# Kernel optimization log

Hardware: AMD Instinct MI355X
Metric: run time of the kernel (lower is better)

Reference implementation:

```python
import jax, jax.numpy as jnp
import numpy as np

EPS = 1e-8
B, H, N, W = 128, 4, 4096, 128


def setup_inputs() -> dict:
    key = jax.random.key(0)
    k1, k2, k3 = jax.random.split(key, 3)
    memory = jax.random.normal(k1, (B, N, W), dtype=jnp.float32)
    controls = jax.random.normal(k2, (B, H * (3 * W + 6)), dtype=jnp.float32)
    write_dist_bias = jax.random.normal(k3, (1, H, N), dtype=jnp.float32) * 10.0
    return {"memory": memory, "controls": controls, "write_dist_bias": write_dist_bias}


def _split_controls(controls):
    # split_tensor: sequential narrows along last dim, each part viewed as [B, H, size]
    sizes = [W, W, W, 1, 1, 3, 1]
    parts, pos = [], 0
    for s in sizes:
        parts.append(controls[:, pos:pos + H * s].reshape(B, H, s))
        pos += H * s
    return parts  # keys, erase, write, betas, gates, shifts, gammas


def _circular_convolution(weights, shifts):
    # out[n] = s0*w[n-1] + s1*w[n] + s2*w[n+1]  (circular)
    return (shifts[..., 0:1] * jnp.roll(weights, 1, axis=-1)
            + shifts[..., 1:2] * weights
            + shifts[..., 2:3] * jnp.roll(weights, -1, axis=-1))


def reference(memory, controls, write_dist_bias):
    keys_r, erase_r, write_r, betas_r, gates_r, shifts_r, gammas_r = _split_controls(controls)

    keys = jnp.tanh(keys_r)                      # [B,H,W]
    betas = jax.nn.softplus(betas_r)             # [B,H,1]
    gates = jax.nn.sigmoid(gates_r)              # [B,H,1]
    shifts = jax.nn.softmax(shifts_r, axis=-1)   # [B,H,3]
    gammas = 1.0 + jax.nn.softplus(gammas_r)     # [B,H,1]

    # cosine distance: [B,H,N]
    dots = jnp.einsum('bnw,bhw->bhn', memory, keys)
    norm = jnp.linalg.norm(keys, axis=-1)[:, :, None] * jnp.linalg.norm(memory, axis=-1)[:, None, :]
    scores = dots / (norm + EPS)

    w_content = jax.nn.softmax(scores * betas, axis=-1)

    # prev weights: first step -> softmax of bias broadcast over batch
    prev_weights = jax.nn.softmax(jnp.broadcast_to(write_dist_bias, (B, H, N)), axis=-1)

    w_interp = gates * w_content + (1.0 - gates) * prev_weights
    w_shift = _circular_convolution(w_interp, shifts)
    w_sharp = w_shift ** gammas
    write_dist = w_sharp / (jnp.sum(w_sharp, axis=-1, keepdims=True) + EPS)  # [B,H,N]

    write_data = jnp.tanh(write_r)        # [B,H,W]
    erase_data = jax.nn.sigmoid(erase_r)  # [B,H,W]

    # erase matrix: prod over heads of (1 - dist x erase) -> [B,N,W]
    erase_matrix = jnp.prod(1.0 - write_dist[:, :, :, None] * erase_data[:, :, None, :], axis=1)
    update_matrix = jnp.einsum('bhn,bhw->bnw', write_dist, write_data)
    return memory * erase_matrix + update_matrix
```

## Files before the change

### kernel.cpp

```cpp
#include <hip/hip_runtime.h>
#include <math.h>

#define B 128
#define H 4
#define N 4096
#define W 128
#define CTRL (H*(3*W+6))
#define EPSF 1e-8f

typedef float f32x4 __attribute__((ext_vector_type(4)));

__device__ __forceinline__ float sigmoidf_(float x){ return 1.0f/(1.0f+expf(-x)); }
__device__ __forceinline__ float softplusf_(float x){ return (x>20.0f)? x : log1pf(expf(x)); }
__device__ __forceinline__ float pospowf_(float t, float g){ return exp2f(g * log2f(t)); }

__device__ __forceinline__ float blockReduceSum256(float v, float* red){
  int tid = threadIdx.x;
  #pragma unroll
  for (int off=32; off>0; off>>=1) v += __shfl_xor(v, off);
  __syncthreads();
  if ((tid&63)==0) red[tid>>6] = v;
  __syncthreads();
  return red[0]+red[1]+red[2]+red[3];
}
__device__ __forceinline__ float blockReduceMax256(float v, float* red){
  int tid = threadIdx.x;
  #pragma unroll
  for (int off=32; off>0; off>>=1) v = fmaxf(v, __shfl_xor(v, off));
  __syncthreads();
  if ((tid&63)==0) red[tid>>6] = v;
  __syncthreads();
  return fmaxf(fmaxf(red[0],red[1]), fmaxf(red[2],red[3]));
}

__global__ __launch_bounds__(128) void prep_kernel(const float* __restrict__ controls,
    float* __restrict__ keys_t, float* __restrict__ erase_s, float* __restrict__ write_t,
    float* __restrict__ scal, const float* __restrict__ bias, float* __restrict__ pw){
  int bid = blockIdx.x;
  int tid = threadIdx.x;
  if (bid >= B*H){
    int h = bid - B*H;
    __shared__ float red2[2];
    const float4* brow = (const float4*)(bias + (size_t)h*N);
    float4 p[8]; float lm = -1e30f;
    #pragma unroll
    for (int j=0;j<8;j++){
      p[j] = brow[tid + 128*j];
      lm = fmaxf(lm, fmaxf(fmaxf(p[j].x,p[j].y), fmaxf(p[j].z,p[j].w)));
    }
    #pragma unroll
    for (int off=32; off>0; off>>=1) lm = fmaxf(lm, __shfl_xor(lm, off));
    if ((tid&63)==0) red2[tid>>6] = lm;
    __syncthreads();
    float m = fmaxf(red2[0], red2[1]);
    float ls = 0.0f;
    #pragma unroll
    for (int j=0;j<8;j++){
      p[j].x = expf(p[j].x-m); p[j].y = expf(p[j].y-m);
      p[j].z = expf(p[j].z-m); p[j].w = expf(p[j].w-m);
      ls += p[j].x+p[j].y+p[j].z+p[j].w;
    }
    #pragma unroll
    for (int off=32; off>0; off>>=1) ls += __shfl_xor(ls, off);
    __syncthreads();
    if ((tid&63)==0) red2[tid>>6] = ls;
    __syncthreads();
    float inv = 1.0f/(red2[0]+red2[1]);
    float4* orow = (float4*)(pw + (size_t)h*N);
    #pragma unroll
    for (int j=0;j<8;j++)
      orow[tid + 128*j] = make_float4(p[j].x*inv, p[j].y*inv, p[j].z*inv, p[j].w*inv);
    return;
  }
  int b = bid >> 2, h = bid & (H-1);
  int w = tid;
  const float* c = controls + (size_t)b*CTRL;
  float k = tanhf(c[h*W + w]);
  keys_t [bid*W + w] = k;
  erase_s[bid*W + w] = sigmoidf_(c[1*H*W + h*W + w]);
  write_t[bid*W + w] = tanhf   (c[2*H*W + h*W + w]);
  __shared__ float red[128];
  red[w] = k*k;
  __syncthreads();
  for (int s=64; s>0; s>>=1){ if (w<s) red[w] += red[w+s]; __syncthreads(); }
  if (w==0){
    float knorm = sqrtf(red[0]);
    float beta  = softplusf_(c[3*H*W + h]);
    float gate  = sigmoidf_ (c[3*H*W + H + h]);
    float s0r = c[3*H*W + 2*H + h*3 + 0];
    float s1r = c[3*H*W + 2*H + h*3 + 1];
    float s2r = c[3*H*W + 2*H + h*3 + 2];
    float mm = fmaxf(s0r, fmaxf(s1r, s2r));
    float e0 = expf(s0r-mm), e1 = expf(s1r-mm), e2 = expf(s2r-mm);
    float inv = 1.0f/(e0+e1+e2);
    float gamma = 1.0f + softplusf_(c[3*H*W + 5*H + h]);
    float* sc = scal + bid*8;
    sc[0]=beta; sc[1]=gate; sc[2]=e0*inv; sc[3]=e1*inv; sc[4]=e2*inv; sc[5]=gamma; sc[6]=knorm;
  }
}

__global__ __launch_bounds__(256) void scores_kernel(const float* __restrict__ memory,
    const float* __restrict__ keys_t, const float* __restrict__ scal,
    float* __restrict__ scores){
  int b = blockIdx.y;
  int n0 = blockIdx.x * 64;
  int tid = threadIdx.x;
  int grp = tid >> 4, l16 = tid & 15;
  __shared__ __align__(16) float kk[H][W];
  __shared__ float kbeta[H], kn[H];
  for (int i = tid; i < H*W; i += 256) kk[0][i] = keys_t[(size_t)b*H*W + i];
  if (tid < H){ kbeta[tid] = scal[(b*H+tid)*8 + 0]; kn[tid] = scal[(b*H+tid)*8 + 6]; }
  __syncthreads();
  float4 ka[H], kb[H];
  #pragma unroll
  for (int h=0;h<H;h++){
    ka[h] = *(const float4*)&kk[h][l16*8];
    kb[h] = *(const float4*)&kk[h][l16*8+4];
  }
  float beta_l = (l16 < H) ? kbeta[l16] : 0.0f;
  float kn_l   = (l16 < H) ? kn[l16]    : 1.0f;
  #pragma unroll
  for (int it=0; it<4; ++it){
    int n = n0 + it*16 + grp;
    const float4* mp = (const float4*)(memory + ((size_t)b*N + n)*W + l16*8);
    float4 ma = mp[0], mb = mp[1];
    float msq = ma.x*ma.x+ma.y*ma.y+ma.z*ma.z+ma.w*ma.w
              + mb.x*mb.x+mb.y*mb.y+mb.z*mb.z+mb.w*mb.w;
    float d0 = ma.x*ka[0].x+ma.y*ka[0].y+ma.z*ka[0].z+ma.w*ka[0].w
             + mb.x*kb[0].x+mb.y*kb[0].y+mb.z*kb[0].z+mb.w*kb[0].w;
    float d1 = ma.x*ka[1].x+ma.y*ka[1].y+ma.z*ka[1].z+ma.w*ka[1].w
             + mb.x*kb[1].x+mb.y*kb[1].y+mb.z*kb[1].z+mb.w*kb[1].w;
    float d2 = ma.x*ka[2].x+ma.y*ka[2].y+ma.z*ka[2].z+ma.w*ka[2].w
             + mb.x*kb[2].x+mb.y*kb[2].y+mb.z*kb[2].z+mb.w*kb[2].w;
    float d3 = ma.x*ka[3].x+ma.y*ka[3].y+ma.z*ka[3].z+ma.w*ka[3].w
             + mb.x*kb[3].x+mb.y*kb[3].y+mb.z*kb[3].z+mb.w*kb[3].w;
    #pragma unroll
    for (int off=1; off<16; off<<=1){
      msq += __shfl_xor(msq, off);
      d0  += __shfl_xor(d0 , off);
      d1  += __shfl_xor(d1 , off);
      d2  += __shfl_xor(d2 , off);
      d3  += __shfl_xor(d3 , off);
    }
    if (l16 < H){
      float dd = (l16==0)?d0 : (l16==1)?d1 : (l16==2)?d2 : d3;
      float mn = sqrtf(msq);
      scores[((size_t)(b*H + l16))*N + n] = beta_l*dd/(kn_l*mn + EPSF);
    }
  }
}

__global__ __launch_bounds__(256) void dist_kernel(const float* scores,
    const float* __restrict__ pw, const float* __restrict__ scal, float* wd){
  int bh = blockIdx.x;
  int h = bh & (H-1);
  int tid = threadIdx.x;
  __shared__ __align__(16) float buf[N];
  __shared__ float red[4];
  const float4* srow4 = (const float4*)(scores + (size_t)bh*N);

  float4 v[4]; float lmax = -1e30f;
  #pragma unroll
  for (int j=0;j<4;j++){
    v[j] = srow4[tid + 256*j];
    lmax = fmaxf(lmax, fmaxf(fmaxf(v[j].x,v[j].y), fmaxf(v[j].z,v[j].w)));
  }
  float smax = blockReduceMax256(lmax, red);
  float lsum = 0.0f;
  #pragma unroll
  for (int j=0;j<4;j++){
    v[j].x = expf(v[j].x-smax); v[j].y = expf(v[j].y-smax);
    v[j].z = expf(v[j].z-smax); v[j].w = expf(v[j].w-smax);
    lsum += v[j].x+v[j].y+v[j].z+v[j].w;
  }
  float ssum = blockReduceSum256(lsum, red);

  float gate = scal[bh*8+1];
  float ga = gate/ssum, gb = 1.0f - gate;
  const float4* prow4 = (const float4*)(pw + (size_t)h*N);
  #pragma unroll
  for (int j=0;j<4;j++){
    float4 p = prow4[tid + 256*j];
    float4 o;
    o.x = ga*v[j].x + gb*p.x;  o.y = ga*v[j].y + gb*p.y;
    o.z = ga*v[j].z + gb*p.z;  o.w = ga*v[j].w + gb*p.w;
    ((float4*)buf)[tid + 256*j] = o;
  }
  __syncthreads();

  float s0 = scal[bh*8+2], s1 = scal[bh*8+3], s2 = scal[bh*8+4], gamma = scal[bh*8+5];
  float4 q[4]; float qsum = 0.0f;
  #pragma unroll
  for (int j=0;j<4;j++){
    int m = 4*(tid + 256*j);
    float4 c = *(const float4*)&buf[m];
    float wm = buf[(m + N - 1) & (N-1)];
    float wp = buf[(m + 4) & (N-1)];
    float t0 = s0*wm  + s1*c.x + s2*c.y;
    float t1 = s0*c.x + s1*c.y + s2*c.z;
    float t2 = s0*c.y + s1*c.z + s2*c.w;
    float t3 = s0*c.z + s1*c.w + s2*wp;
    q[j].x = pospowf_(t0, gamma); q[j].y = pospowf_(t1, gamma);
    q[j].z = pospowf_(t2, gamma); q[j].w = pospowf_(t3, gamma);
    qsum += q[j].x+q[j].y+q[j].z+q[j].w;
  }
  float tot = blockReduceSum256(qsum, red);
  float inv = 1.0f/(tot + EPSF);
  float4* wrow4 = (float4*)(wd + (size_t)bh*N);
  #pragma unroll
  for (int j=0;j<4;j++)
    wrow4[tid + 256*j] = make_float4(q[j].x*inv, q[j].y*inv, q[j].z*inv, q[j].w*inv);
}

__global__ __launch_bounds__(256) void final_kernel(const float* __restrict__ memory,
    const float* __restrict__ wd, const float* __restrict__ erase_s,
    const float* __restrict__ write_t, float* __restrict__ out){
  int b  = (B-1) - blockIdx.y;
  int n0 = ((N/64-1) - blockIdx.x) * 64;
  int tid = threadIdx.x;
  __shared__ __align__(16) float esh[H][W];
  __shared__ __align__(16) float wsh[H][W];
  __shared__ float wdsh[H][64];
  for (int i=tid;i<H*W;i+=256){ esh[0][i] = erase_s[(size_t)b*H*W+i]; wsh[0][i] = write_t[(size_t)b*H*W+i]; }
  for (int i=tid;i<H*64;i+=256){ int h=i>>6, r=i&63; wdsh[h][r] = wd[((size_t)(b*H+h))*N + n0 + r]; }
  __syncthreads();
  int wq = (tid & 31) * 4;
  int rl = tid >> 5;
  #pragma unroll
  for (int rr = 0; rr < 8; ++rr){
    int r = rl + rr*8;
    int n = n0 + r;
    size_t base = ((size_t)b*N + n)*W + wq;
    f32x4 m = __builtin_nontemporal_load((const f32x4*)(memory + base));
    float px=1.f, py=1.f, pz=1.f, pwv=1.f;
    float ux=0.f, uy=0.f, uz=0.f, uw=0.f;
    #pragma unroll
    for (int h=0;h<H;h++){
      float d = wdsh[h][r];
      float4 e  = *(const float4*)&esh[h][wq];
      float4 wv = *(const float4*)&wsh[h][wq];
      px *= 1.0f - d*e.x;  py *= 1.0f - d*e.y;
      pz *= 1.0f - d*e.z;  pwv*= 1.0f - d*e.w;
      ux += d*wv.x;  uy += d*wv.y;  uz += d*wv.z;  uw += d*wv.w;
    }
    f32x4 o;
    o.x = m.x*px + ux;  o.y = m.y*py + uy;
    o.z = m.z*pz + uz;  o.w = m.w*pwv + uw;
    __builtin_nontemporal_store(o, (f32x4*)(out + base));
  }
}

extern "C" void kernel_launch(void* const* d_in, const int* in_sizes, int n_in,
                              void* d_out, int out_size, void* d_ws, size_t ws_size,
                              hipStream_t stream){
  const float* memory   = (const float*)d_in[0];
  const float* controls = (const float*)d_in[1];
  const float* bias     = (const float*)d_in[2];
  float* out = (float*)d_out;

  float* ws      = (float*)d_ws;
  float* keys_t  = ws;
  float* erase_s = keys_t  + B*H*W;
  float* write_t = erase_s + B*H*W;
  float* scal    = write_t + B*H*W;
  float* pw      = scal    + B*H*8;
  float* scores  = pw      + H*N;
  float* wd      = scores;

  prep_kernel  <<<dim3(B*H + H),  dim3(128), 0, stream>>>(controls, keys_t, erase_s, write_t, scal, bias, pw);
  scores_kernel<<<dim3(N/64, B),  dim3(256), 0, stream>>>(memory, keys_t, scal, scores);
  dist_kernel  <<<dim3(B*H),      dim3(256), 0, stream>>>(scores, pw, scal, wd);
  final_kernel <<<dim3(N/64, B),  dim3(256), 0, stream>>>(memory, wd, erase_s, write_t, out);
}
```

Before: 498.5 us.

## Fuse write-distribution and memory-update kernels into one 1024-thread kernel

Merges dist_kernel and final_kernel into one kernel launched on a grid of 2 by B blocks of 1024 threads. Each block recomputes the full write distribution for all four heads of its batch in shared memory (64KB) and then updates half of the memory rows. This removes one launch and the global write and read of the distribution, at the cost of doing the softmax, shift and sharpen work twice per batch. It also cuts the grid to 256 large blocks, which may limit occupancy and latency hiding during the bandwidth-bound update phase.

```diff
diff --git a/kernel.cpp b/kernel.cpp
--- a/kernel.cpp
+++ b/kernel.cpp
@@ -14,23 +14,29 @@
 __device__ __forceinline__ float softplusf_(float x){ return (x>20.0f)? x : log1pf(expf(x)); }
 __device__ __forceinline__ float pospowf_(float t, float g){ return exp2f(g * log2f(t)); }
 
-__device__ __forceinline__ float blockReduceSum256(float v, float* red){
+__device__ __forceinline__ float blockReduceSum1024(float v, float* red){
   int tid = threadIdx.x;
   #pragma unroll
   for (int off=32; off>0; off>>=1) v += __shfl_xor(v, off);
   __syncthreads();
   if ((tid&63)==0) red[tid>>6] = v;
   __syncthreads();
-  return red[0]+red[1]+red[2]+red[3];
-}
-__device__ __forceinline__ float blockReduceMax256(float v, float* red){
+  float s = 0.0f;
+  #pragma unroll
+  for (int i=0;i<16;i++) s += red[i];
+  return s;
+}
+__device__ __forceinline__ float blockReduceMax1024(float v, float* red){
   int tid = threadIdx.x;
   #pragma unroll
   for (int off=32; off>0; off>>=1) v = fmaxf(v, __shfl_xor(v, off));
   __syncthreads();
   if ((tid&63)==0) red[tid>>6] = v;
   __syncthreads();
-  return fmaxf(fmaxf(red[0],red[1]), fmaxf(red[2],red[3]));
+  float s = -1e30f;
+  #pragma unroll
+  for (int i=0;i<16;i++) s = fmaxf(s, red[i]);
+  return s;
 }
 
 __global__ __launch_bounds__(128) void prep_kernel(const float* __restrict__ controls,
@@ -150,102 +156,87 @@
   }
 }
 
-__global__ __launch_bounds__(256) void dist_kernel(const float* scores,
-    const float* __restrict__ pw, const float* __restrict__ scal, float* wd){
-  int bh = blockIdx.x;
-  int h = bh & (H-1);
-  int tid = threadIdx.x;
-  __shared__ __align__(16) float buf[N];
-  __shared__ float red[4];
-  const float4* srow4 = (const float4*)(scores + (size_t)bh*N);
-
-  float4 v[4]; float lmax = -1e30f;
-  #pragma unroll
-  for (int j=0;j<4;j++){
-    v[j] = srow4[tid + 256*j];
-    lmax = fmaxf(lmax, fmaxf(fmaxf(v[j].x,v[j].y), fmaxf(v[j].z,v[j].w)));
-  }
-  float smax = blockReduceMax256(lmax, red);
-  float lsum = 0.0f;
-  #pragma unroll
-  for (int j=0;j<4;j++){
-    v[j].x = expf(v[j].x-smax); v[j].y = expf(v[j].y-smax);
-    v[j].z = expf(v[j].z-smax); v[j].w = expf(v[j].w-smax);
-    lsum += v[j].x+v[j].y+v[j].z+v[j].w;
-  }
-  float ssum = blockReduceSum256(lsum, red);
-
-  float gate = scal[bh*8+1];
-  float ga = gate/ssum, gb = 1.0f - gate;
-  const float4* prow4 = (const float4*)(pw + (size_t)h*N);
-  #pragma unroll
-  for (int j=0;j<4;j++){
-    float4 p = prow4[tid + 256*j];
+__global__ __launch_bounds__(1024) void fused_kernel(const float* __restrict__ memory,
+    const float* __restrict__ scores, const float* __restrict__ pw,
+    const float* __restrict__ scal, const float* __restrict__ erase_s,
+    const float* __restrict__ write_t, float* __restrict__ out){
+  int b = (B-1) - blockIdx.y;
+  int q = blockIdx.x;
+  int tid = threadIdx.x;
+  __shared__ float wd_sh[H][N];
+  __shared__ __align__(16) float esh[H][W];
+  __shared__ __align__(16) float wsh[H][W];
+  __shared__ float red[16];
+  for (int i=tid;i<H*W;i+=1024){
+    esh[0][i] = erase_s[(size_t)b*H*W+i];
+    wsh[0][i] = write_t[(size_t)b*H*W+i];
+  }
+
+  #pragma unroll
+  for (int h=0; h<H; h++){
+    const float4* srow = (const float4*)(scores + ((size_t)(b*H+h))*N);
+    float4 v = srow[tid];
+    float lm = fmaxf(fmaxf(v.x,v.y), fmaxf(v.z,v.w));
+    float smax = blockReduceMax1024(lm, red);
+    v.x = expf(v.x-smax); v.y = expf(v.y-smax);
+    v.z = expf(v.z-smax); v.w = expf(v.w-smax);
+    float ssum = blockReduceSum1024(v.x+v.y+v.z+v.w, red);
+    float gate = scal[(b*H+h)*8+1];
+    float ga = gate/ssum, gb = 1.0f - gate;
+    float4 p = ((const float4*)(pw + (size_t)h*N))[tid];
     float4 o;
-    o.x = ga*v[j].x + gb*p.x;  o.y = ga*v[j].y + gb*p.y;
-    o.z = ga*v[j].z + gb*p.z;  o.w = ga*v[j].w + gb*p.w;
-    ((float4*)buf)[tid + 256*j] = o;
-  }
-  __syncthreads();
-
-  float s0 = scal[bh*8+2], s1 = scal[bh*8+3], s2 = scal[bh*8+4], gamma = scal[bh*8+5];
-  float4 q[4]; float qsum = 0.0f;
-  #pragma unroll
-  for (int j=0;j<4;j++){
-    int m = 4*(tid + 256*j);
-    float4 c = *(const float4*)&buf[m];
-    float wm = buf[(m + N - 1) & (N-1)];
-    float wp = buf[(m + 4) & (N-1)];
+    o.x = ga*v.x + gb*p.x;  o.y = ga*v.y + gb*p.y;
+    o.z = ga*v.z + gb*p.z;  o.w = ga*v.w + gb*p.w;
+    ((float4*)wd_sh[h])[tid] = o;
+  }
+  __syncthreads();
+
+  #pragma unroll
+  for (int h=0; h<H; h++){
+    float s0 = scal[(b*H+h)*8+2], s1 = scal[(b*H+h)*8+3];
+    float s2 = scal[(b*H+h)*8+4], g  = scal[(b*H+h)*8+5];
+    int m = 4*tid;
+    float4 c = *(const float4*)&wd_sh[h][m];
+    float wm = wd_sh[h][(m + N - 1) & (N-1)];
+    float wp = wd_sh[h][(m + 4) & (N-1)];
     float t0 = s0*wm  + s1*c.x + s2*c.y;
     float t1 = s0*c.x + s1*c.y + s2*c.z;
     float t2 = s0*c.y + s1*c.z + s2*c.w;
     float t3 = s0*c.z + s1*c.w + s2*wp;
-    q[j].x = pospowf_(t0, gamma); q[j].y = pospowf_(t1, gamma);
-    q[j].z = pospowf_(t2, gamma); q[j].w = pospowf_(t3, gamma);
-    qsum += q[j].x+q[j].y+q[j].z+q[j].w;
-  }
-  float tot = blockReduceSum256(qsum, red);
-  float inv = 1.0f/(tot + EPSF);
-  float4* wrow4 = (float4*)(wd + (size_t)bh*N);
-  #pragma unroll
-  for (int j=0;j<4;j++)
-    wrow4[tid + 256*j] = make_float4(q[j].x*inv, q[j].y*inv, q[j].z*inv, q[j].w*inv);
-}
-
-__global__ __launch_bounds__(256) void final_kernel(const float* __restrict__ memory,
-    const float* __restrict__ wd, const float* __restrict__ erase_s,
-    const float* __restrict__ write_t, float* __restrict__ out){
-  int b  = (B-1) - blockIdx.y;
-  int n0 = ((N/64-1) - blockIdx.x) * 64;
-  int tid = threadIdx.x;
-  __shared__ __align__(16) float esh[H][W];
-  __shared__ __align__(16) float wsh[H][W];
-  __shared__ float wdsh[H][64];
-  for (int i=tid;i<H*W;i+=256){ esh[0][i] = erase_s[(size_t)b*H*W+i]; wsh[0][i] = write_t[(size_t)b*H*W+i]; }
-  for (int i=tid;i<H*64;i+=256){ int h=i>>6, r=i&63; wdsh[h][r] = wd[((size_t)(b*H+h))*N + n0 + r]; }
-  __syncthreads();
-  int wq = (tid & 31) * 4;
-  int rl = tid >> 5;
-  #pragma unroll
-  for (int rr = 0; rr < 8; ++rr){
-    int r = rl + rr*8;
-    int n = n0 + r;
-    size_t base = ((size_t)b*N + n)*W + wq;
+    float q0 = pospowf_(t0,g), q1 = pospowf_(t1,g);
+    float q2 = pospowf_(t2,g), q3 = pospowf_(t3,g);
+    float tot = blockReduceSum1024(q0+q1+q2+q3, red);
+    float inv = 1.0f/(tot + EPSF);
+    *(float4*)&wd_sh[h][m] = make_float4(q0*inv, q1*inv, q2*inv, q3*inv);
+  }
+  __syncthreads();
+
+  int col = tid & 31;
+  int rg  = tid >> 5;
+  f32x4 ev[H], wv[H];
+  #pragma unroll
+  for (int h=0;h<H;h++){
+    ev[h] = *(const f32x4*)&esh[h][col*4];
+    wv[h] = *(const f32x4*)&wsh[h][col*4];
+  }
+  int nbase = q*(N/2);
+  #pragma unroll 4
+  for (int rr=0; rr<64; ++rr){
+    int n = nbase + rr*32 + rg;
+    size_t base = ((size_t)b*N + n)*W + col*4;
     f32x4 m = __builtin_nontemporal_load((const f32x4*)(memory + base));
-    float px=1.f, py=1.f, pz=1.f, pwv=1.f;
+    float px=1.f, py=1.f, pz=1.f, pq=1.f;
     float ux=0.f, uy=0.f, uz=0.f, uw=0.f;
     #pragma unroll
     for (int h=0;h<H;h++){
-      float d = wdsh[h][r];
-      float4 e  = *(const float4*)&esh[h][wq];
-      float4 wv = *(const float4*)&wsh[h][wq];
-      px *= 1.0f - d*e.x;  py *= 1.0f - d*e.y;
-      pz *= 1.0f - d*e.z;  pwv*= 1.0f - d*e.w;
-      ux += d*wv.x;  uy += d*wv.y;  uz += d*wv.z;  uw += d*wv.w;
+      float d = wd_sh[h][n];
+      px *= 1.0f - d*ev[h].x;  py *= 1.0f - d*ev[h].y;
+      pz *= 1.0f - d*ev[h].z;  pq *= 1.0f - d*ev[h].w;
+      ux += d*wv[h].x;  uy += d*wv[h].y;  uz += d*wv[h].z;  uw += d*wv[h].w;
     }
     f32x4 o;
     o.x = m.x*px + ux;  o.y = m.y*py + uy;
-    o.z = m.z*pz + uz;  o.w = m.w*pwv + uw;
+    o.z = m.z*pz + uz;  o.w = m.w*pq + uw;
     __builtin_nontemporal_store(o, (f32x4*)(out + base));
   }
 }
@@ -265,10 +256,8 @@
   float* scal    = write_t + B*H*W;
   float* pw      = scal    + B*H*8;
   float* scores  = pw      + H*N;
-  float* wd      = scores;
-
-  prep_kernel  <<<dim3(B*H + H),  dim3(128), 0, stream>>>(controls, keys_t, erase_s, write_t, scal, bias, pw);
-  scores_kernel<<<dim3(N/64, B),  dim3(256), 0, stream>>>(memory, keys_t, scal, scores);
-  dist_kernel  <<<dim3(B*H),      dim3(256), 0, stream>>>(scores, pw, scal, wd);
-  final_kernel <<<dim3(N/64, B),  dim3(256), 0, stream>>>(memory, wd, erase_s, write_t, out);
-}
+
+  prep_kernel  <<<dim3(B*H + H),  dim3(128),  0, stream>>>(controls, keys_t, erase_s, write_t, scal, bias, pw);
+  scores_kernel<<<dim3(N/64, B),  dim3(256),  0, stream>>>(memory, keys_t, scal, scores);
+  fused_kernel <<<dim3(2, B),     dim3(1024), 0, stream>>>(memory, scores, pw, scal, erase_s, write_t, out);
+}
```

Result: slower. 514.6 us (+3.2%).
